# Optimization experiments

Hardware: AMD Instinct MI355X
Metric: run time of the kernel (lower is better)

## Reference

```python
import jax, jax.numpy as jnp
import numpy as np
from jax import lax

HEADS = 8
DIM_HEAD = 64
SCALE = DIM_HEAD ** -0.5

def conv2d(x, w, stride=1, pad=0):
    return lax.conv_general_dilated(
        x, w, window_strides=(stride, stride),
        padding=[(pad, pad), (pad, pad)],
        dimension_numbers=("NCHW", "OIHW", "NCHW"))

def setup_inputs() -> dict:
    key = jax.random.key(0)
    ks = jax.random.split(key, 5)
    b, dim, H, W = 8, 256, 32, 32
    inner = HEADS * DIM_HEAD  # 512
    x = jax.random.normal(ks[0], (b, dim, H, W), jnp.float32)
    Wq = jax.random.normal(ks[1], (inner, dim, 1, 1), jnp.float32) * 0.05
    Wkv = jax.random.normal(ks[2], (2 * inner, dim, 3, 3), jnp.float32) * 0.05
    Wout = jax.random.normal(ks[3], (dim, inner, 1, 1), jnp.float32) * 0.05
    bout = jnp.zeros((dim,), jnp.float32)
    return {"x": x, "Wq": Wq, "Wkv": Wkv, "Wout": Wout, "bout": bout}

def reference(x, Wq, Wkv, Wout, bout):
    b = x.shape[0]
    h, d = HEADS, DIM_HEAD
    q = conv2d(x, Wq, stride=1, pad=0)        # [b, h*d, H, W]
    kv = conv2d(x, Wkv, stride=1, pad=1)      # [b, 2*h*d, H, W]
    k, v = jnp.split(kv, 2, axis=1)
    out_h, out_w = q.shape[-2:]

    def to_bhnd(t):
        # b (h d) x y -> b h (x y) d
        B, _, X, Y = t.shape
        return t.reshape(B, h, d, X * Y).transpose(0, 1, 3, 2)

    q, k, v = map(to_bhnd, (q, k, v))
    dots = jnp.einsum("bhid,bhjd->bhij", q, k) * SCALE
    attn = jax.nn.softmax(dots, axis=-1)
    out = jnp.einsum("bhij,bhjd->bhid", attn, v)  # [b, h, n, d]
    # b h (x y) d -> b (h d) x y
    out = out.transpose(0, 1, 3, 2).reshape(b, h * d, out_h, out_w)
    out = jax.nn.gelu(out, approximate=False)
    out = conv2d(out, Wout, stride=1, pad=0) + bout[None, :, None, None]
    return out
```

## Files before the change

### kernel.cpp

```cpp
#include <hip/hip_runtime.h>
#include <math.h>

#define BATCH 8
#define DIM   256
#define NPIX  1024
#define DHEAD 64
#define INNER 512
#define KVCH  1024

typedef _Float16 half8 __attribute__((ext_vector_type(8)));
typedef _Float16 half4 __attribute__((ext_vector_type(4)));
typedef float    f32x4 __attribute__((ext_vector_type(4)));
#define MFMA16(a, b, c) __builtin_amdgcn_mfma_f32_16x16x32_f16(a, b, c, 0, 0, 0)

static __device__ __forceinline__ float gelu_f(float v) {
    return 0.5f * v * (1.0f + erff(v * 0.70710678118654752440f));
}

static __device__ __forceinline__ void gload16(const _Float16* g, _Float16* l) {
    __builtin_amdgcn_global_load_lds(
        (const __attribute__((address_space(1))) unsigned int*)g,
        (__attribute__((address_space(3))) unsigned int*)l, 16, 0, 0);
}

__global__ __launch_bounds__(256) void prep_w_kernel(
    const float* __restrict__ Wq, const float* __restrict__ Wkv,
    const float* __restrict__ Wout, _Float16* __restrict__ Aq,
    _Float16* __restrict__ Akv, _Float16* __restrict__ Aout)
{
    const int e = blockIdx.x * 256 + threadIdx.x;
    if (e < 131072) Aq[e] = (_Float16)Wq[e];
    const int e2 = e - 131072;
    if (e2 >= 0 && e2 < 2359296) {
        int oc = e2 / 2304, r = e2 - oc * 2304;
        int s = r >> 8, ic = r & 255;
        Akv[e2] = (_Float16)Wkv[oc * 2304 + ic * 9 + s];
    }
    const int e3 = e - 131072 - 2359296;
    if (e3 >= 0 && e3 < 131072) Aout[e3] = (_Float16)Wout[e3];
}

__global__ __launch_bounds__(256) void transpose_x_kernel(
    const float* __restrict__ x, _Float16* __restrict__ xt)
{
    __shared__ float ts[64][65];
    const int pt = blockIdx.x * 64, ic0 = blockIdx.y * 64, b = blockIdx.z;
    const int tid = threadIdx.x;
    const float* xb = x + (((size_t)(b * DIM + ic0)) << 10) + pt;
#pragma unroll
    for (int e = tid; e < 4096; e += 256) {
        int i = e >> 6, p = e & 63;
        ts[i][p] = xb[((size_t)i << 10) + p];
    }
    __syncthreads();
#pragma unroll
    for (int e = tid; e < 4096; e += 256) {
        int p = e >> 6, i = e & 63;
        xt[((size_t)(b * NPIX + pt + p)) * 256 + ic0 + i] = (_Float16)ts[i][p];
    }
}

template<int M, int K, int KROW, bool SHIFT, int EPI>
__global__ __launch_bounds__(256) void gemm_kernel(
    const _Float16* __restrict__ A, const _Float16* __restrict__ act,
    const _Float16* __restrict__ zbuf, void* __restrict__ Cout,
    void* __restrict__ CoutB, const float* __restrict__ bias)
{
    __shared__ _Float16 As[128 * 64];
    __shared__ _Float16 Bs[128 * 64];
    const int nt = blockIdx.x, mt = blockIdx.y, b = blockIdx.z;
    const int tid = threadIdx.x;
    const int w = tid >> 6, lane = tid & 63;
    const int quad = lane >> 4, l15 = lane & 15;
    const int m0 = mt * 128, p0 = nt * 128;
    const int wm = (w >> 1) * 64, wn = (w & 1) * 64;
    const f32x4 Z4 = {0.f, 0.f, 0.f, 0.f};

    const int srow = lane >> 3;
    const int scol = ((lane & 7) ^ srow) * 8;

    int prow[4];
    const _Float16* agp[4];
#pragma unroll
    for (int c = 0; c < 4; ++c) {
        int row = (w * 4 + c) * 8 + srow;
        prow[c] = row;
        agp[c] = A + (size_t)(m0 + row) * K + scol;
    }

    f32x4 acc[4][4];
#pragma unroll
    for (int mi = 0; mi < 4; ++mi)
#pragma unroll
        for (int ni = 0; ni < 4; ++ni) acc[mi][ni] = Z4;

    for (int kt = 0; kt < K / 64; ++kt) {
        __syncthreads();
#pragma unroll
        for (int c = 0; c < 4; ++c)
            gload16(agp[c] + kt * 64, &As[(w * 4 + c) * 512]);
        if (!SHIFT) {
#pragma unroll
            for (int c = 0; c < 4; ++c)
                gload16(act + (size_t)(b * NPIX + p0 + prow[c]) * KROW + kt * 64 + scol,
                        &Bs[(w * 4 + c) * 512]);
        } else {
            const int s  = kt >> 2;
            const int dy = s / 3 - 1;
            const int dx = s - (s / 3) * 3 - 1;
            const int icb = (kt & 3) * 64 + scol;
#pragma unroll
            for (int c = 0; c < 4; ++c) {
                int p  = p0 + prow[c];
                int py = p >> 5, px = p & 31;
                bool ok = ((unsigned)(py + dy) < 32u) && ((unsigned)(px + dx) < 32u);
                const _Float16* gp = ok
                    ? act + (size_t)(b * NPIX + p + dy * 32 + dx) * 256 + icb
                    : zbuf;
                gload16(gp, &Bs[(w * 4 + c) * 512]);
            }
        }
        __syncthreads();
#pragma unroll
        for (int ks = 0; ks < 2; ++ks) {
            half8 av[4], bv[4];
#pragma unroll
            for (int mi = 0; mi < 4; ++mi) {
                const int r = wm + mi * 16 + l15;
                av[mi] = *(const half8*)&As[r * 64 + (((ks * 4 + quad) ^ (l15 & 7)) << 3)];
            }
#pragma unroll
            for (int ni = 0; ni < 4; ++ni) {
                const int r = wn + ni * 16 + l15;
                bv[ni] = *(const half8*)&Bs[r * 64 + (((ks * 4 + quad) ^ (l15 & 7)) << 3)];
            }
#pragma unroll
            for (int mi = 0; mi < 4; ++mi)
#pragma unroll
                for (int ni = 0; ni < 4; ++ni)
                    acc[mi][ni] = MFMA16(av[mi], bv[ni], acc[mi][ni]);
        }
    }

    if (EPI <= 1) {
#pragma unroll
        for (int mi = 0; mi < 4; ++mi) {
#pragma unroll
            for (int r = 0; r < 4; ++r) {
                const int m = m0 + wm + mi * 16 + quad * 4 + r;
                const float bv = (EPI == 1) ? bias[m] : 0.f;
#pragma unroll
                for (int ni = 0; ni < 4; ++ni) {
                    const int pix = p0 + wn + ni * 16 + l15;
                    if (EPI == 0) {
                        ((_Float16*)Cout)[(((size_t)(b * M + m)) << 10) + pix] =
                            (_Float16)acc[mi][ni][r];
                    } else {
                        ((float*)Cout)[(((size_t)(b * M + m)) << 10) + pix] =
                            acc[mi][ni][r] + bv;
                    }
                }
            }
        }
    } else {
#pragma unroll
        for (int mi = 0; mi < 4; ++mi) {
            const int mbase = m0 + wm + mi * 16;
            if (EPI == 3 && mbase >= 512) {
#pragma unroll
                for (int r = 0; r < 4; ++r) {
                    const int mv = mbase + quad * 4 + r - 512;
#pragma unroll
                    for (int ni = 0; ni < 4; ++ni) {
                        const int pix = p0 + wn + ni * 16 + l15;
                        ((_Float16*)Cout)[(((size_t)(b * 512 + mv)) << 10) + pix] =
                            (_Float16)acc[mi][ni][r];
                    }
                }
            } else {
                const int h  = mbase >> 6;
                const int dd = (mbase & 63) + quad * 4;
                _Float16* dst = (EPI == 2) ? (_Float16*)Cout : (_Float16*)CoutB;
#pragma unroll
                for (int ni = 0; ni < 4; ++ni) {
                    const int pix = p0 + wn + ni * 16 + l15;
                    half4 v4;
#pragma unroll
                    for (int r = 0; r < 4; ++r) {
                        float vv = acc[mi][ni][r];
                        if (EPI == 2) vv *= 0.125f;
                        v4[r] = (_Float16)vv;
                    }
                    *(half4*)&dst[((((size_t)(b * 8 + h)) << 10) + pix) * 64 + dd] = v4;
                }
            }
        }
    }
}

__global__ __launch_bounds__(256) void attn_kernel(
    const _Float16* __restrict__ qt,
    const _Float16* __restrict__ ktp,
    const _Float16* __restrict__ vbb,
    _Float16* __restrict__ gout)
{
    __shared__ _Float16 Ks[128 * 64];
    __shared__ _Float16 Vs[64 * 128];
    __shared__ _Float16 Pb[128 * 128];
    const int qtile = blockIdx.x, bh = blockIdx.y;
    const int b = bh >> 3, h = bh & 7;
    const int p0 = qtile * 128;
    const int tid = threadIdx.x;
    const int w = tid >> 6, lane = tid & 63;
    const int quad = lane >> 4, l15 = lane & 15;
    const f32x4 Z4 = {0.f, 0.f, 0.f, 0.f};

    half8 ones;
#pragma unroll
    for (int u = 0; u < 8; ++u) ones[u] = (_Float16)1.0f;

    half8 qf[2][2];
    {
        const _Float16* qrow =
            qt + ((((size_t)(bh)) << 10) + p0 + w * 32 + l15) * 64;
#pragma unroll
        for (int iff = 0; iff < 2; ++iff)
#pragma unroll
            for (int ks = 0; ks < 2; ++ks)
                qf[iff][ks] = *(const half8*)(qrow + iff * 16 * 64 + ks * 32 + quad * 8);
    }

    const _Float16* kbase = ktp + ((size_t)bh << 16);
    const _Float16* vbase = vbb + (((size_t)(b * 512 + h * 64)) << 10);

    f32x4 oacc[4][2];
#pragma unroll
    for (int mf = 0; mf < 4; ++mf)
#pragma unroll
        for (int iff = 0; iff < 2; ++iff) oacc[mf][iff] = Z4;
    f32x4 racc[2] = {Z4, Z4};

    const int kchunk = (lane & 7) ^ (lane >> 3);
    for (int kt = 0; kt < 8; ++kt) {
        const int pk = kt * 128;
        __syncthreads();
        const _Float16* kg = kbase + (size_t)pk * 64;
#pragma unroll
        for (int i = 0; i < 4; ++i) {
            const int t = i * 4 + w;
            gload16(kg + (t * 8 + (lane >> 3)) * 64 + kchunk * 8, &Ks[t * 512]);
        }
#pragma unroll
        for (int i = 0; i < 4; ++i) {
            const int t = i * 4 + w;
            const int vd = t * 4 + (lane >> 4);
            gload16(vbase + ((size_t)vd << 10) + pk + (((lane & 15) ^ (vd & 15)) << 3),
                    &Vs[t * 512]);
        }
        __syncthreads();

#pragma unroll
        for (int g = 0; g < 2; ++g) {
            f32x4 s[4][2];
#pragma unroll
            for (int jf2 = 0; jf2 < 4; ++jf2) {
                const int jr = (g * 4 + jf2) * 16 + l15;
                const half8 ka0 = *(const half8*)&Ks[jr * 64 + ((quad ^ (l15 & 7)) << 3)];
                const half8 ka1 = *(const half8*)&Ks[jr * 64 + (((4 + quad) ^ (l15 & 7)) << 3)];
#pragma unroll
                for (int iff = 0; iff < 2; ++iff) {
                    s[jf2][iff] = MFMA16(ka0, qf[iff][0], Z4);
                    s[jf2][iff] = MFMA16(ka1, qf[iff][1], s[jf2][iff]);
                }
            }
#pragma unroll
            for (int jf2 = 0; jf2 < 4; ++jf2) {
#pragma unroll
                for (int iff = 0; iff < 2; ++iff) {
                    half4 pv4;
#pragma unroll
                    for (int r = 0; r < 4; ++r)
                        pv4[r] = (_Float16)__expf(s[jf2][iff][r] - 8.0f);
                    const int i = w * 32 + iff * 16 + l15;
                    const int c = ((g * 4 + jf2) << 1) + (quad >> 1);
                    *(half4*)&Pb[i * 128 + ((c ^ l15) << 3) + ((quad & 1) << 2)] = pv4;
                }
            }
        }
#pragma unroll
        for (int kc = 0; kc < 4; ++kc) {
            half8 bv[2];
#pragma unroll
            for (int iff = 0; iff < 2; ++iff) {
                const int i = w * 32 + iff * 16 + l15;
                bv[iff] = *(const half8*)&Pb[i * 128 + (((kc * 4 + quad) ^ l15) << 3)];
                racc[iff] = MFMA16(ones, bv[iff], racc[iff]);
            }
#pragma unroll
            for (int mf = 0; mf < 4; ++mf) {
                const int vr = mf * 16 + l15;
                const half8 va = *(const half8*)&Vs[vr * 128 + (((kc * 4 + quad) ^ l15) << 3)];
#pragma unroll
                for (int iff = 0; iff < 2; ++iff)
                    oacc[mf][iff] = MFMA16(va, bv[iff], oacc[mf][iff]);
            }
        }
    }

    float rinv[2];
#pragma unroll
    for (int iff = 0; iff < 2; ++iff) rinv[iff] = 1.f / racc[iff][0];

    __syncthreads();
    _Float16* scr = Pb;
#pragma unroll
    for (int mf = 0; mf < 4; ++mf) {
#pragma unroll
        for (int iff = 0; iff < 2; ++iff) {
            half4 o4;
#pragma unroll
            for (int r = 0; r < 4; ++r)
                o4[r] = (_Float16)gelu_f(oacc[mf][iff][r] * rinv[iff]);
            const int i = w * 32 + iff * 16 + l15;
            *(half4*)&scr[i * 72 + mf * 16 + quad * 4] = o4;
        }
    }
    __syncthreads();
    _Float16* go = gout + ((size_t)(b * NPIX + p0)) * INNER + h * 64;
#pragma unroll
    for (int it = 0; it < 4; ++it) {
        const int e = tid + it * 256;
        const int p = e >> 3, dg = e & 7;
        *(half8*)(go + (size_t)p * INNER + dg * 8) = *(const half8*)&scr[p * 72 + dg * 8];
    }
}

extern "C" void kernel_launch(void* const* d_in, const int* in_sizes, int n_in,
                              void* d_out, int out_size, void* d_ws, size_t ws_size,
                              hipStream_t stream)
{
    const float* x    = (const float*)d_in[0];
    const float* Wq   = (const float*)d_in[1];
    const float* Wkv  = (const float*)d_in[2];
    const float* Wout = (const float*)d_in[3];
    const float* bout = (const float*)d_in[4];
    float* out = (float*)d_out;

    _Float16* zbuf = (_Float16*)d_ws;
    _Float16* Aout = zbuf + 256;
    _Float16* xt   = Aout + (size_t)DIM * INNER;
    _Float16* Aq   = xt   + (size_t)BATCH * NPIX * DIM;
    _Float16* Akv  = Aq   + (size_t)INNER * DIM;
    _Float16* qt   = Akv  + (size_t)KVCH * 2304;
    _Float16* vb   = qt   + (size_t)BATCH * NPIX * INNER;
    _Float16* ktp  = vb   + (size_t)BATCH * NPIX * INNER;
    _Float16* gout = ktp  + (size_t)BATCH * NPIX * INNER;

    (void)hipMemsetAsync(zbuf, 0, 512, stream);

    prep_w_kernel<<<10240, 256, 0, stream>>>(Wq, Wkv, Wout, Aq, Akv, Aout);
    transpose_x_kernel<<<dim3(16, 4, BATCH), 256, 0, stream>>>(x, xt);
    gemm_kernel<INNER, 256, 256, false, 2>
        <<<dim3(8, 4, BATCH), 256, 0, stream>>>(Aq, xt, zbuf, qt, nullptr, nullptr);
    gemm_kernel<KVCH, 2304, 256, true, 3>
        <<<dim3(8, 8, BATCH), 256, 0, stream>>>(Akv, xt, zbuf, vb, ktp, nullptr);
    attn_kernel<<<dim3(8, 64), 256, 0, stream>>>(qt, ktp, vb, gout);
    gemm_kernel<DIM, 512, 512, false, 1>
        <<<dim3(8, 2, BATCH), 256, 0, stream>>>(Aout, gout, zbuf, out, nullptr, bout);
}
```

Baseline: 188.6 us.

## Fuse Q and KV convolutions into one GEMM over zero-padded input

Measured after the change: 192.2 us. About the same (+1.9%).

```diff
diff --git a/kernel.cpp b/kernel.cpp
--- a/kernel.cpp
+++ b/kernel.cpp
@@ -7,6 +7,7 @@
 #define DHEAD 64
 #define INNER 512
 #define KVCH  1024
+#define PPIX  1156
 
 typedef _Float16 half8 __attribute__((ext_vector_type(8)));
 typedef _Float16 half4 __attribute__((ext_vector_type(4)));
@@ -41,7 +42,7 @@
 }
 
 __global__ __launch_bounds__(256) void transpose_x_kernel(
-    const float* __restrict__ x, _Float16* __restrict__ xt)
+    const float* __restrict__ x, _Float16* __restrict__ xtp)
 {
     __shared__ float ts[64][65];
     const int pt = blockIdx.x * 64, ic0 = blockIdx.y * 64, b = blockIdx.z;
@@ -54,17 +55,125 @@
     }
     __syncthreads();
 #pragma unroll
-    for (int e = tid; e < 4096; e += 256) {
-        int p = e >> 6, i = e & 63;
-        xt[((size_t)(b * NPIX + pt + p)) * 256 + ic0 + i] = (_Float16)ts[i][p];
-    }
-}
-
-template<int M, int K, int KROW, bool SHIFT, int EPI>
-__global__ __launch_bounds__(256) void gemm_kernel(
+    for (int e = tid; e < 512; e += 256) {
+        int p = e >> 3, ig = e & 7;
+        int gp = pt + p, y = gp >> 5, xc = gp & 31;
+        half8 v;
+#pragma unroll
+        for (int u = 0; u < 8; ++u) v[u] = (_Float16)ts[ig * 8 + u][p];
+        *(half8*)&xtp[((size_t)b * PPIX + (y + 1) * 34 + xc + 1) * 256 + ic0 + ig * 8] = v;
+    }
+}
+
+__global__ __launch_bounds__(256) void qkv_gemm_kernel(
+    const _Float16* __restrict__ Akv, const _Float16* __restrict__ Aq,
+    const _Float16* __restrict__ xtp, _Float16* __restrict__ qt,
+    _Float16* __restrict__ ktp, _Float16* __restrict__ vb)
+{
+    __shared__ _Float16 As[128 * 64];
+    __shared__ _Float16 Bs[128 * 64];
+    const int nt = blockIdx.x, mt = blockIdx.y, b = blockIdx.z;
+    const bool QBLK = (mt >= 8);
+    const int tid = threadIdx.x;
+    const int w = tid >> 6, lane = tid & 63;
+    const int quad = lane >> 4, l15 = lane & 15;
+    const int m0 = (QBLK ? mt - 8 : mt) * 128, p0 = nt * 128;
+    const int wm = (w >> 1) * 64, wn = (w & 1) * 64;
+    const f32x4 Z4 = {0.f, 0.f, 0.f, 0.f};
+
+    const int srow = lane >> 3;
+    const int scol = ((lane & 7) ^ srow) * 8;
+
+    const _Float16* abase = QBLK ? Aq : Akv;
+    const int astride = QBLK ? 256 : 2304;
+    const int ktend = QBLK ? 4 : 36;
+
+    const _Float16* agp[4];
+    const _Float16* bgp[4];
+#pragma unroll
+    for (int c = 0; c < 4; ++c) {
+        int row = (w * 4 + c) * 8 + srow;
+        agp[c] = abase + (size_t)(m0 + row) * astride + scol;
+        int p = p0 + row, py = p >> 5, px = p & 31;
+        bgp[c] = xtp + ((size_t)b * PPIX + (py + 1) * 34 + px + 1) * 256 + scol;
+    }
+
+    f32x4 acc[4][4];
+#pragma unroll
+    for (int mi = 0; mi < 4; ++mi)
+#pragma unroll
+        for (int ni = 0; ni < 4; ++ni) acc[mi][ni] = Z4;
+
+    for (int kt = 0; kt < ktend; ++kt) {
+        __syncthreads();
+        const int s = QBLK ? 4 : (kt >> 2);
+        const int doff = (s / 3 - 1) * 34 + (s - (s / 3) * 3) - 1;
+        const int boff = doff * 256 + (kt & 3) * 64;
+#pragma unroll
+        for (int c = 0; c < 4; ++c)
+            gload16(agp[c] + kt * 64, &As[(w * 4 + c) * 512]);
+#pragma unroll
+        for (int c = 0; c < 4; ++c)
+            gload16(bgp[c] + boff, &Bs[(w * 4 + c) * 512]);
+        __syncthreads();
+#pragma unroll
+        for (int ks = 0; ks < 2; ++ks) {
+            half8 av[4], bv[4];
+#pragma unroll
+            for (int mi = 0; mi < 4; ++mi) {
+                const int r = wm + mi * 16 + l15;
+                av[mi] = *(const half8*)&As[r * 64 + (((ks * 4 + quad) ^ (l15 & 7)) << 3)];
+            }
+#pragma unroll
+            for (int ni = 0; ni < 4; ++ni) {
+                const int r = wn + ni * 16 + l15;
+                bv[ni] = *(const half8*)&Bs[r * 64 + (((ks * 4 + quad) ^ (l15 & 7)) << 3)];
+            }
+#pragma unroll
+            for (int mi = 0; mi < 4; ++mi)
+#pragma unroll
+                for (int ni = 0; ni < 4; ++ni)
+                    acc[mi][ni] = MFMA16(av[mi], bv[ni], acc[mi][ni]);
+        }
+    }
+
+#pragma unroll
+    for (int mi = 0; mi < 4; ++mi) {
+        const int mbase = m0 + wm + mi * 16;
+        if (!QBLK && mbase >= 512) {
+#pragma unroll
+            for (int r = 0; r < 4; ++r) {
+                const int mv = mbase + quad * 4 + r - 512;
+#pragma unroll
+                for (int ni = 0; ni < 4; ++ni) {
+                    const int pix = p0 + wn + ni * 16 + l15;
+                    vb[(((size_t)(b * 512 + mv)) << 10) + pix] = (_Float16)acc[mi][ni][r];
+                }
+            }
+        } else {
+            const int h  = mbase >> 6;
+            const int dd = (mbase & 63) + quad * 4;
+            _Float16* dst = QBLK ? qt : ktp;
+#pragma unroll
+            for (int ni = 0; ni < 4; ++ni) {
+                const int pix = p0 + wn + ni * 16 + l15;
+                half4 v4;
+#pragma unroll
+                for (int r = 0; r < 4; ++r) {
+                    float vv = acc[mi][ni][r];
+                    if (QBLK) vv *= 0.125f;
+                    v4[r] = (_Float16)vv;
+                }
+                *(half4*)&dst[((((size_t)(b * 8 + h)) << 10) + pix) * 64 + dd] = v4;
+            }
+        }
+    }
+}
+
+template<int M, int K, int KROW>
+__global__ __launch_bounds__(256) void out_gemm_kernel(
     const _Float16* __restrict__ A, const _Float16* __restrict__ act,
-    const _Float16* __restrict__ zbuf, void* __restrict__ Cout,
-    void* __restrict__ CoutB, const float* __restrict__ bias)
+    float* __restrict__ Cout, const float* __restrict__ bias)
 {
     __shared__ _Float16 As[128 * 64];
     __shared__ _Float16 Bs[128 * 64];
@@ -99,27 +208,10 @@
 #pragma unroll
         for (int c = 0; c < 4; ++c)
             gload16(agp[c] + kt * 64, &As[(w * 4 + c) * 512]);
-        if (!SHIFT) {
-#pragma unroll
-            for (int c = 0; c < 4; ++c)
-                gload16(act + (size_t)(b * NPIX + p0 + prow[c]) * KROW + kt * 64 + scol,
-                        &Bs[(w * 4 + c) * 512]);
-        } else {
-            const int s  = kt >> 2;
-            const int dy = s / 3 - 1;
-            const int dx = s - (s / 3) * 3 - 1;
-            const int icb = (kt & 3) * 64 + scol;
-#pragma unroll
-            for (int c = 0; c < 4; ++c) {
-                int p  = p0 + prow[c];
-                int py = p >> 5, px = p & 31;
-                bool ok = ((unsigned)(py + dy) < 32u) && ((unsigned)(px + dx) < 32u);
-                const _Float16* gp = ok
-                    ? act + (size_t)(b * NPIX + p + dy * 32 + dx) * 256 + icb
-                    : zbuf;
-                gload16(gp, &Bs[(w * 4 + c) * 512]);
-            }
-        }
+#pragma unroll
+        for (int c = 0; c < 4; ++c)
+            gload16(act + (size_t)(b * NPIX + p0 + prow[c]) * KROW + kt * 64 + scol,
+                    &Bs[(w * 4 + c) * 512]);
         __syncthreads();
 #pragma unroll
         for (int ks = 0; ks < 2; ++ks) {
@@ -142,57 +234,16 @@
         }
     }
 
-    if (EPI <= 1) {
-#pragma unroll
-        for (int mi = 0; mi < 4; ++mi) {
-#pragma unroll
-            for (int r = 0; r < 4; ++r) {
-                const int m = m0 + wm + mi * 16 + quad * 4 + r;
-                const float bv = (EPI == 1) ? bias[m] : 0.f;
-#pragma unroll
-                for (int ni = 0; ni < 4; ++ni) {
-                    const int pix = p0 + wn + ni * 16 + l15;
-                    if (EPI == 0) {
-                        ((_Float16*)Cout)[(((size_t)(b * M + m)) << 10) + pix] =
-                            (_Float16)acc[mi][ni][r];
-                    } else {
-                        ((float*)Cout)[(((size_t)(b * M + m)) << 10) + pix] =
-                            acc[mi][ni][r] + bv;
-                    }
-                }
-            }
-        }
-    } else {
-#pragma unroll
-        for (int mi = 0; mi < 4; ++mi) {
-            const int mbase = m0 + wm + mi * 16;
-            if (EPI == 3 && mbase >= 512) {
-#pragma unroll
-                for (int r = 0; r < 4; ++r) {
-                    const int mv = mbase + quad * 4 + r - 512;
-#pragma unroll
-                    for (int ni = 0; ni < 4; ++ni) {
-                        const int pix = p0 + wn + ni * 16 + l15;
-                        ((_Float16*)Cout)[(((size_t)(b * 512 + mv)) << 10) + pix] =
-                            (_Float16)acc[mi][ni][r];
-                    }
-                }
-            } else {
-                const int h  = mbase >> 6;
-                const int dd = (mbase & 63) + quad * 4;
-                _Float16* dst = (EPI == 2) ? (_Float16*)Cout : (_Float16*)CoutB;
-#pragma unroll
-                for (int ni = 0; ni < 4; ++ni) {
-                    const int pix = p0 + wn + ni * 16 + l15;
-                    half4 v4;
-#pragma unroll
-                    for (int r = 0; r < 4; ++r) {
-                        float vv = acc[mi][ni][r];
-                        if (EPI == 2) vv *= 0.125f;
-                        v4[r] = (_Float16)vv;
-                    }
-                    *(half4*)&dst[((((size_t)(b * 8 + h)) << 10) + pix) * 64 + dd] = v4;
-                }
+#pragma unroll
+    for (int mi = 0; mi < 4; ++mi) {
+#pragma unroll
+        for (int r = 0; r < 4; ++r) {
+            const int m = m0 + wm + mi * 16 + quad * 4 + r;
+            const float bv = bias[m];
+#pragma unroll
+            for (int ni = 0; ni < 4; ++ni) {
+                const int pix = p0 + wn + ni * 16 + l15;
+                Cout[(((size_t)(b * M + m)) << 10) + pix] = acc[mi][ni][r] + bv;
             }
         }
     }
@@ -346,25 +397,21 @@
     const float* bout = (const float*)d_in[4];
     float* out = (float*)d_out;
 
-    _Float16* zbuf = (_Float16*)d_ws;
-    _Float16* Aout = zbuf + 256;
-    _Float16* xt   = Aout + (size_t)DIM * INNER;
-    _Float16* Aq   = xt   + (size_t)BATCH * NPIX * DIM;
+    _Float16* xtp  = (_Float16*)d_ws;
+    _Float16* Aq   = xtp  + (size_t)BATCH * PPIX * DIM;
     _Float16* Akv  = Aq   + (size_t)INNER * DIM;
-    _Float16* qt   = Akv  + (size_t)KVCH * 2304;
+    _Float16* Aout = Akv  + (size_t)KVCH * 2304;
+    _Float16* qt   = Aout + (size_t)DIM * INNER;
     _Float16* vb   = qt   + (size_t)BATCH * NPIX * INNER;
     _Float16* ktp  = vb   + (size_t)BATCH * NPIX * INNER;
     _Float16* gout = ktp  + (size_t)BATCH * NPIX * INNER;
 
-    (void)hipMemsetAsync(zbuf, 0, 512, stream);
+    (void)hipMemsetAsync(xtp, 0, (size_t)BATCH * PPIX * DIM * sizeof(_Float16), stream);
 
     prep_w_kernel<<<10240, 256, 0, stream>>>(Wq, Wkv, Wout, Aq, Akv, Aout);
-    transpose_x_kernel<<<dim3(16, 4, BATCH), 256, 0, stream>>>(x, xt);
-    gemm_kernel<INNER, 256, 256, false, 2>
-        <<<dim3(8, 4, BATCH), 256, 0, stream>>>(Aq, xt, zbuf, qt, nullptr, nullptr);
-    gemm_kernel<KVCH, 2304, 256, true, 3>
-        <<<dim3(8, 8, BATCH), 256, 0, stream>>>(Akv, xt, zbuf, vb, ktp, nullptr);
+    transpose_x_kernel<<<dim3(16, 4, BATCH), 256, 0, stream>>>(x, xtp);
+    qkv_gemm_kernel<<<dim3(8, 12, BATCH), 256, 0, stream>>>(Akv, Aq, xtp, qt, ktp, vb);
     attn_kernel<<<dim3(8, 64), 256, 0, stream>>>(qt, ktp, vb, gout);
-    gemm_kernel<DIM, 512, 512, false, 1>
-        <<<dim3(8, 2, BATCH), 256, 0, stream>>>(Aout, gout, zbuf, out, nullptr, bout);
-}
+    out_gemm_kernel<DIM, 512, 512>
+        <<<dim3(8, 2, BATCH), 256, 0, stream>>>(Aout, gout, out, bout);
+}
```
